# Optimization experiments

Hardware: AMD Instinct MI355X
Metric: run time of the kernel (lower is better)

## Reference

```python
import jax, jax.numpy as jnp
import numpy as np

V, H, L, BW = 32000, 512, 2, 5   # vocab, hidden(=embed), gru layers, beam width
NEG = -1e9                        # -inf surrogate for duplicate initial beams


def gru_cell(x, h, Wi, Wh, bi, bh):
    # PyTorch GRU gate order: r, z, n.  x:[B,H] h:[B,H] Wi,Wh:[3H,H]
    gi = x @ Wi.T + bi
    gh = h @ Wh.T + bh
    ir, iz, inn = jnp.split(gi, 3, axis=-1)
    hr, hz, hn = jnp.split(gh, 3, axis=-1)
    r = jax.nn.sigmoid(ir + hr)
    z = jax.nn.sigmoid(iz + hz)
    n = jnp.tanh(inn + r * hn)
    return (1.0 - z) * n + z * h


def setup_inputs() -> dict:
    key = jax.random.key(0)
    ks = jax.random.split(key, 14)
    s = 0.05
    p = lambda k, shape: jax.random.normal(k, shape, jnp.float32) * s
    return {
        "input_seq": jax.random.randint(ks[0], (128, 1), 0, V),
        "input_length": 128,
        "max_length": 64,
        "SOS_token": 1,
        "emb": p(ks[1], (V, H)),
        "enc_Wi": p(ks[2], (L, 3 * H, H)),
        "enc_Wh": p(ks[3], (L, 3 * H, H)),
        "enc_bi": p(ks[4], (L, 3 * H)),
        "enc_bh": p(ks[5], (L, 3 * H)),
        "dec_Wi": p(ks[6], (L, 3 * H, H)),
        "dec_Wh": p(ks[7], (L, 3 * H, H)),
        "dec_bi": p(ks[8], (L, 3 * H)),
        "dec_bh": p(ks[9], (L, 3 * H)),
        "Wc": p(ks[10], (H, 2 * H)),
        "bc": p(ks[11], (H,)),
        "Wout": p(ks[12], (V, H)),
        "bout": p(ks[13], (V,)),
    }


def reference(input_seq, input_length, max_length, SOS_token,
              emb, enc_Wi, enc_Wh, enc_bi, enc_bh,
              dec_Wi, dec_Wh, dec_bi, dec_bh, Wc, bc, Wout, bout):
    # ---- encoder: L-layer GRU over [T,1] token ids ----
    x = emb[input_seq[:, 0]]                    # [T,H]

    def enc_step(h, xt):                        # h:[L,1,H]
        inp = xt[None]                          # [1,H]
        hs = []
        for l in range(L):
            hl = gru_cell(inp, h[l], enc_Wi[l], enc_Wh[l], enc_bi[l], enc_bh[l])
            hs.append(hl)
            inp = hl
        return jnp.stack(hs), inp[0]

    h0 = jnp.zeros((L, 1, H), x.dtype)
    enc_hidden, enc_out = jax.lax.scan(enc_step, h0, x)   # enc_out:[T,H]

    # ---- one decoder step, batched over all BW beams ----
    def dec_step(tokens, hidden):               # tokens:[BW] hidden:[L,BW,H]
        inp = emb[tokens]                       # [BW,H]
        hs = []
        for l in range(L):
            hl = gru_cell(inp, hidden[l], dec_Wi[l], dec_Wh[l], dec_bi[l], dec_bh[l])
            hs.append(hl)
            inp = hl
        rnn = inp                               # [BW,H] top-layer output
        e = jnp.einsum('bh,th->bt', rnn, enc_out)          # Luong dot scores
        a = jax.nn.softmax(e, axis=-1)
        ctx = a @ enc_out                       # [BW,H]
        cc = jnp.tanh(jnp.concatenate([rnn, ctx], axis=-1) @ Wc.T + bc)
        logits = cc @ Wout.T + bout             # [BW,V]
        return logits, jnp.stack(hs)

    # ---- beam search: all beams in one batched decoder call per step ----
    tokens0 = jnp.full((BW,), SOS_token, jnp.int32)
    hid0 = jnp.broadcast_to(enc_hidden, (L, BW, H))
    scores0 = jnp.full((BW,), NEG, jnp.float32).at[0].set(0.0)  # one live beam

    def step(carry, _):
        tokens, hidden, scores = carry
        logits, hidden = dec_step(tokens, hidden)
        logp = jax.nn.log_softmax(logits, axis=-1)
        top_lp, top_idx = jax.lax.top_k(logp, BW)            # [BW,BW]
        cand = (scores[:, None] + top_lp).reshape(-1)        # [BW*BW]
        sc, flat = jax.lax.top_k(cand, BW)
        parent = flat // BW
        new_tok = top_idx.reshape(-1)[flat]
        hidden = hidden[:, parent, :]
        return (new_tok, hidden, sc), (new_tok, parent)

    (_, _, final_scores), (toks, pars) = jax.lax.scan(
        step, (tokens0, hid0, scores0), None, length=max_length)

    # ---- backtrack best hypothesis through parent pointers ----
    best = jnp.argmax(final_scores)

    def back(beam, tp):
        t, p = tp
        return p[beam], t[beam]

    _, seq = jax.lax.scan(back, best, (toks, pars), reverse=True)
    return seq, final_scores[best]
```

## Files before the change

kernel.cpp:

```cpp
#include <hip/hip_runtime.h>
#include <math.h>

#define VV 32000
#define HH 512
#define G3 1536
#define TI 128
#define TO 64
#define NB 5
#define NEGF (-1000000000.0f)
#define NTHR 256
#define NT5 512
#define NCH 500
#define LSTR 32

struct Params {
  const int* seq;
  const int* sosp;
  const float *emb, *eWi, *eWh, *ebi, *ebh;
  const float *dWi, *dWh, *dbi, *dbh;
  const float *Wc, *bc, *Wout, *bout;
  unsigned* bar;
  int *cur_tok, *toks, *pars, *ptop_i;
  float *gi0, *eout, *h0b, *h1b, *dch, *cc, *ptop_v, *psum, *scores;
  float* out;
};

__device__ __forceinline__ float cldf(const float* p) {
  return __hip_atomic_load(p, __ATOMIC_RELAXED, __HIP_MEMORY_SCOPE_AGENT);
}
__device__ __forceinline__ void cstf(float* p, float v) {
  __hip_atomic_store(p, v, __ATOMIC_RELAXED, __HIP_MEMORY_SCOPE_AGENT);
}
__device__ __forceinline__ int cldi(const int* p) {
  return __hip_atomic_load(p, __ATOMIC_RELAXED, __HIP_MEMORY_SCOPE_AGENT);
}
__device__ __forceinline__ void csti(int* p, int v) {
  __hip_atomic_store(p, v, __ATOMIC_RELAXED, __HIP_MEMORY_SCOPE_AGENT);
}
__device__ __forceinline__ unsigned rldu(const unsigned* p) {
  return __hip_atomic_load(p, __ATOMIC_RELAXED, __HIP_MEMORY_SCOPE_AGENT);
}
typedef unsigned long long u64t;
union F2U { u64t u; float f[2]; };
__device__ __forceinline__ void cld2(float* d, const float* p) {
  F2U x; x.u = __hip_atomic_load((const u64t*)p, __ATOMIC_RELAXED, __HIP_MEMORY_SCOPE_AGENT);
  d[0] = x.f[0]; d[1] = x.f[1];
}

__device__ __forceinline__ void bar_arrive(unsigned* lines, int myline) {
  __syncthreads();
  if (threadIdx.x == 0)
    __hip_atomic_fetch_add(lines + myline * LSTR, 1u,
                           __ATOMIC_RELAXED, __HIP_MEMORY_SCOPE_AGENT);
}
template <int SLP>
__device__ __forceinline__ void bar_wait8(const unsigned* lines, unsigned tgt) {
  if (threadIdx.x < 64) {
    for (;;) {
      unsigned v = tgt;
      if (threadIdx.x < 8) v = rldu(lines + threadIdx.x * LSTR);
      if (__all(v >= tgt)) break;
      __builtin_amdgcn_s_sleep(SLP);
    }
  }
  __syncthreads();
}
__device__ __forceinline__ void bcast_store(unsigned* L, int NL, unsigned tok) {
  asm volatile("s_waitcnt vmcnt(0)" ::: "memory");
  for (int i = 0; i < NL; i++)
    __hip_atomic_store(L + i * LSTR, tok, __ATOMIC_RELAXED, __HIP_MEMORY_SCOPE_AGENT);
}
template <int SLP>
__device__ __forceinline__ void leaf_wait(const unsigned* L, int grp, unsigned tok) {
  if (threadIdx.x == 0) {
    while (rldu(L + grp * LSTR) < tok) __builtin_amdgcn_s_sleep(SLP);
  }
  __syncthreads();
}

__device__ __forceinline__ float wredf(float v) {
#pragma unroll
  for (int o = 32; o; o >>= 1) v += __shfl_xor(v, o, 64);
  return v;
}

__global__ void __launch_bounds__(NTHR) k_e0(Params p) {
  const int wg = blockIdx.x, tid = threadIdx.x;
  const int lane = tid & 63, wv = tid >> 6;
  if (wg == 0) {
    for (int i = tid; i < 2 * HH; i += NTHR) { cstf(&p.h0b[i], 0.f); cstf(&p.h1b[i], 0.f); }
  }
  for (int lr = 0; lr < 6; lr++) {
    int row = wg * 6 + lr;
    const float* W = p.eWi + (size_t)row * HH;
    float w0[8];
#pragma unroll
    for (int j = 0; j < 8; j++) w0[j] = W[j * 64 + lane];
    float bi = p.ebi[row];
    for (int t = wv; t < TI; t += 4) {
      const float* x = p.emb + (size_t)p.seq[t] * HH;
      float s = 0.f;
#pragma unroll
      for (int j = 0; j < 8; j++) s += w0[j] * x[j * 64 + lane];
      s = wredf(s);
      if (lane == 0) p.gi0[(size_t)t * G3 + row] = s + bi;
    }
  }
}

__device__ void enc_step(const Params& p, int T, int wg, int lane, int wv) {
  const int sIn = T & 1, sOut = sIn ^ 1;
  if (wv < 2) {
    if (T < TI) {
      float hv[8];
#pragma unroll
      for (int j = 0; j < 8; j++) hv[j] = cldf(&p.h0b[sIn * HH + j * 64 + lane]);
#pragma unroll
      for (int uu = 0; uu < 4; uu++) {
        int u = wg * 8 + wv * 4 + uu;
        float g[3];
#pragma unroll
        for (int gg = 0; gg < 3; gg++) {
          const float* W = p.eWh + (size_t)(gg * HH + u) * HH;
          float s = 0.f;
#pragma unroll
          for (int j = 0; j < 8; j++) s += W[j * 64 + lane] * hv[j];
          g[gg] = wredf(s);
        }
        if (lane == 0) {
          const float* gr = p.gi0 + (size_t)T * G3;
          float ir = gr[u], iz = gr[HH + u], inn = gr[2 * HH + u];
          float hr = g[0] + p.ebh[u], hz = g[1] + p.ebh[HH + u], hn = g[2] + p.ebh[2 * HH + u];
          float r = 1.f / (1.f + expf(-(ir + hr)));
          float z = 1.f / (1.f + expf(-(iz + hz)));
          float n = tanhf(inn + r * hn);
          float hp = cldf(&p.h0b[sIn * HH + u]);
          cstf(&p.h0b[sOut * HH + u], (1.f - z) * n + z * hp);
        }
      }
    }
  } else {
    if (T >= 1) {
      float xv[8], hv[8];
#pragma unroll
      for (int j = 0; j < 8; j++) {
        xv[j] = cldf(&p.h0b[sIn * HH + j * 64 + lane]);
        hv[j] = cldf(&p.h1b[sOut * HH + j * 64 + lane]);
      }
#pragma unroll
      for (int uu = 0; uu < 4; uu++) {
        int u = wg * 8 + (wv - 2) * 4 + uu;
        float gi[3], gh[3];
#pragma unroll
        for (int gg = 0; gg < 3; gg++) {
          const float* Wi1 = p.eWi + (size_t)G3 * HH + (size_t)(gg * HH + u) * HH;
          const float* Wh1 = p.eWh + (size_t)G3 * HH + (size_t)(gg * HH + u) * HH;
          float si = 0.f, s2 = 0.f;
#pragma unroll
          for (int j = 0; j < 8; j++) { si += Wi1[j * 64 + lane] * xv[j]; s2 += Wh1[j * 64 + lane] * hv[j]; }
          gi[gg] = wredf(si);
          gh[gg] = wredf(s2);
        }
        if (lane == 0) {
          const float* bi = p.ebi + G3;
          const float* bh = p.ebh + G3;
          float ir = gi[0] + bi[u], iz = gi[1] + bi[HH + u], inn = gi[2] + bi[2 * HH + u];
          float hr = gh[0] + bh[u], hz = gh[1] + bh[HH + u], hn = gh[2] + bh[2 * HH + u];
          float r = 1.f / (1.f + expf(-(ir + hr)));
          float z = 1.f / (1.f + expf(-(iz + hz)));
          float n = tanhf(inn + r * hn);
          float hp = cldf(&p.h1b[sOut * HH + u]);
          float hnew = (1.f - z) * n + z * hp;
          cstf(&p.h1b[sIn * HH + u], hnew);
          p.eout[(size_t)(T - 1) * HH + u] = hnew;
        }
      }
    }
  }
}

__global__ void __launch_bounds__(NTHR) k_e1x2(Params p, int k) {
  const int wg = blockIdx.x, tid = threadIdx.x;
  const int lane = tid & 63, wv = tid >> 6;
  unsigned* ceA = p.bar + 0 * LSTR;
  enc_step(p, 2 * k, wg, lane, wv);
  if (2 * k + 1 <= TI) {
    bar_arrive(ceA, wg & 7);
    bar_wait8<2>(ceA, (unsigned)(8 * (k + 1)));
    enc_step(p, 2 * k + 1, wg, lane, wv);
  }
}

__global__ void __launch_bounds__(NTHR) k_d0(Params p) {
  const int wg = blockIdx.x, tid = threadIdx.x;
  for (int i = tid + wg * NTHR; i < 2 * NB * HH; i += 64 * NTHR) {
    int l = i / (NB * HH);
    int rem = i - l * (NB * HH);
    int u = rem % HH;
    p.dch[(size_t)l * NB * HH + rem] = (l == 0) ? cldf(&p.h0b[u]) : cldf(&p.h1b[u]);
  }
  if (wg == 0 && tid < NB) {
    p.cur_tok[tid] = p.sosp[0];
    p.scores[tid] = (tid == 0) ? 0.f : NEGF;
  }
}

template <int LAYER>
__device__ void gru_body(const Params& p, float* sm, int t, int ib, int ob,
                         int wg, int tid, int lane, int wv) {
  float* sx = sm;
  float* sh = sm + NB * HH;
  float* fres = sm + 2 * NB * HH;
  int ct[NB], pr[NB];
#pragma unroll
  for (int b = 0; b < NB; b++) {
    ct[b] = (LAYER == 0) ? cldi(&p.cur_tok[b]) : 0;
    pr[b] = (t == 0) ? b : cldi(&p.pars[(t - 1) * NB + b]);
  }
  for (int i = tid; i < NB * (HH / 2); i += NTHR) {
    int b = i >> 8, c = (i & 255) << 1;
    float x2[2], h2[2];
    if (LAYER == 0) {
      const float* e = p.emb + (size_t)ct[b] * HH + c;
      x2[0] = e[0]; x2[1] = e[1];
    } else {
      cld2(x2, &p.dch[((size_t)(ob * 2 + 0) * NB + b) * HH + c]);
    }
    cld2(h2, &p.dch[((size_t)(ib * 2 + LAYER) * NB + pr[b]) * HH + c]);
    sx[b * HH + c] = x2[0]; sx[b * HH + c + 1] = x2[1];
    sh[b * HH + c] = h2[0]; sh[b * HH + c + 1] = h2[1];
  }
  __syncthreads();
  const float* Wi = p.dWi + (size_t)LAYER * G3 * HH;
  const float* Wh = p.dWh + (size_t)LAYER * G3 * HH;
#pragma unroll
  for (int k = 0; k < 12; k++) {
    const int m_ = k % 6;
    const int f = wv * 12 + k;
    const int ul = f / 6;
    const int u = wg * 8 + ul;
    const float* W = (m_ >= 3 ? Wh : Wi) + (size_t)((m_ % 3) * HH + u) * HH;
    const float* vecb = (m_ >= 3) ? sh : sx;
    float wd[8];
#pragma unroll
    for (int j = 0; j < 8; j++) wd[j] = W[j * 64 + lane];
    float a0 = 0.f, a1 = 0.f, a2 = 0.f, a3 = 0.f, a4 = 0.f;
#pragma unroll
    for (int j = 0; j < 8; j++) {
      float wj = wd[j];
      int o = j * 64 + lane;
      a0 += wj * vecb[0 * HH + o];
      a1 += wj * vecb[1 * HH + o];
      a2 += wj * vecb[2 * HH + o];
      a3 += wj * vecb[3 * HH + o];
      a4 += wj * vecb[4 * HH + o];
    }
    float r0 = wredf(a0), r1 = wredf(a1), r2 = wredf(a2), r3 = wredf(a3), r4 = wredf(a4);
    if (lane == 0) {
      fres[f * NB + 0] = r0; fres[f * NB + 1] = r1; fres[f * NB + 2] = r2;
      fres[f * NB + 3] = r3; fres[f * NB + 4] = r4;
    }
  }
  __syncthreads();
  if (tid < 8 * NB) {
    int ul = tid / NB, b = tid - ul * NB;
    int u = wg * 8 + ul;
    const float* bi = p.dbi + LAYER * G3;
    const float* bh = p.dbh + LAYER * G3;
    float ir = fres[(ul * 6 + 0) * NB + b] + bi[u];
    float iz = fres[(ul * 6 + 1) * NB + b] + bi[HH + u];
    float inn = fres[(ul * 6 + 2) * NB + b] + bi[2 * HH + u];
    float hr = fres[(ul * 6 + 3) * NB + b] + bh[u];
    float hz = fres[(ul * 6 + 4) * NB + b] + bh[HH + u];
    float hn = fres[(ul * 6 + 5) * NB + b] + bh[2 * HH + u];
    float hp = sh[b * HH + u];
    float r = 1.f / (1.f + expf(-(ir + hr)));
    float z = 1.f / (1.f + expf(-(iz + hz)));
    float n = tanhf(inn + r * hn);
    cstf(&p.dch[((size_t)(ob * 2 + LAYER) * NB + b) * HH + u], (1.f - z) * n + z * hp);
  }
  __syncthreads();
}

__global__ void __launch_bounds__(NTHR) k_gru2(Params p, int t) {
  const int wg = blockIdx.x, tid = threadIdx.x;
  const int lane = tid & 63, wv = tid >> 6;
  const int ib = t & 1, ob = ib ^ 1;
  __shared__ float sm[2 * NB * HH + 48 * NB];
  unsigned* gruA = p.bar + 8 * LSTR;
  gru_body<0>(p, sm, t, ib, ob, wg, tid, lane, wv);
  bar_arrive(gruA, wg & 7);
  bar_wait8<2>(gruA, (unsigned)(8 * (t + 1)));
  gru_body<1>(p, sm, t, ib, ob, wg, tid, lane, wv);
}

__global__ void __launch_bounds__(NT5) k_pa56(Params p, int t) {
  const int wg = blockIdx.x, tid = threadIdx.x;
  const int lane = tid & 63, wv = tid >> 6;
  const int ob = (t & 1) ^ 1;
  __shared__ float sm[5760];
  __shared__ unsigned s_mrg;
  unsigned* paA = p.bar + 16 * LSTR;
  unsigned* paF = p.bar + 24 * LSTR;
  unsigned* c5A = p.bar + 48 * LSTR;
  unsigned* c5F = p.bar + 56 * LSTR;
  unsigned* paL = p.bar + 64 * LSTR;

  if (wg < 40) {
    const int b = wg / 8, q = wg % 8;
    float* srnn = sm;
    float* sp = sm + 512;
    float* cpart = sm + 640;
    float* sctx = sm + 4736;
    for (int i = tid; i < HH; i += NT5)
      srnn[i] = cldf(&p.dch[((size_t)(ob * 2 + 1) * NB + b) * HH + i]);
    __syncthreads();
    for (int j = wv; j < TI; j += 8) {
      const float* E = p.eout + (size_t)j * HH;
      float s = 0.f;
#pragma unroll
      for (int k2 = 0; k2 < 8; k2++) s += srnn[k2 * 64 + lane] * E[k2 * 64 + lane];
      s = wredf(s);
      if (lane == 0) sp[j] = s;
    }
    __syncthreads();
    if (wv == 0) {
      float v0 = sp[lane], v1 = sp[64 + lane];
      float mx = fmaxf(v0, v1);
#pragma unroll
      for (int o = 32; o; o >>= 1) mx = fmaxf(mx, __shfl_xor(mx, o, 64));
      float e0 = expf(v0 - mx), e1 = expf(v1 - mx);
      float ss = wredf(e0 + e1);
      sp[lane] = e0 / ss;
      sp[64 + lane] = e1 / ss;
    }
    __syncthreads();
    {
      float cp[8];
#pragma unroll
      for (int k2 = 0; k2 < 8; k2++) cp[k2] = 0.f;
      for (int j = wv; j < TI; j += 8) {
        float spj = sp[j];
        const float* E = p.eout + (size_t)j * HH;
#pragma unroll
        for (int k2 = 0; k2 < 8; k2++) cp[k2] += spj * E[k2 * 64 + lane];
      }
#pragma unroll
      for (int k2 = 0; k2 < 8; k2++) cpart[wv * HH + k2 * 64 + lane] = cp[k2];
    }
    __syncthreads();
    for (int i = tid; i < HH; i += NT5)
      sctx[i] = ((cpart[0 * HH + i] + cpart[1 * HH + i]) + (cpart[2 * HH + i] + cpart[3 * HH + i]))
              + ((cpart[4 * HH + i] + cpart[5 * HH + i]) + (cpart[6 * HH + i] + cpart[7 * HH + i]));
    __syncthreads();
    for (int k = wv; k < 64; k += 8) {
      int u = q * 64 + k;
      const float* W = p.Wc + (size_t)u * (2 * HH);
      float s0 = 0.f, s1 = 0.f;
#pragma unroll
      for (int j = 0; j < 8; j++) {
        int o = j * 64 + lane;
        s0 += W[o] * srnn[o];
        s1 += W[HH + o] * sctx[o];
      }
      float r0 = wredf(s0), r1 = wredf(s1);
      if (lane == 0) cstf(&p.cc[b * HH + u], tanhf(r0 + r1 + p.bc[u]));
    }
    __syncthreads();
    if (tid == 0) {
      unsigned o1 = __hip_atomic_fetch_add(paA + (wg & 7) * LSTR, 1u,
                                           __ATOMIC_RELAXED, __HIP_MEMORY_SCOPE_AGENT);
      if (o1 == (unsigned)(5 * (t + 1) - 1)) {
        unsigned o2 = __hip_atomic_fetch_add(paF, 1u,
                                             __ATOMIC_RELAXED, __HIP_MEMORY_SCOPE_AGENT);
        if (o2 == (unsigned)(8 * (t + 1) - 1))
          bcast_store(paL, 32, (unsigned)(t + 1));
      }
    }
  }
  leaf_wait<4>(paL, wg >> 4, (unsigned)(t + 1));

  {
    float* scc = sm;
    float* slg = sm + 2560;
    float* part = sm + 2944;
    for (int i = tid; i < NB * (HH / 2); i += NT5) {
      int b = i >> 8, c = (i & 255) << 1;
      float c2v[2];
      cld2(c2v, &p.cc[b * HH + c]);
      scc[b * HH + c] = c2v[0]; scc[b * HH + c + 1] = c2v[1];
    }
    __syncthreads();
    const int vbase = wg * 64;
    {
      const int e = tid >> 6, r = tid & 63;
      const float4* Wr = (const float4*)(p.Wout + (size_t)(vbase + r) * HH + e * 64);
      const float* sc0 = scc + e * 64;
      float a0 = 0.f, a1 = 0.f, a2 = 0.f, a3 = 0.f, a4 = 0.f;
#pragma unroll
      for (int c = 0; c < 16; c++) {
        float4 w = Wr[c];
        const float4 s0 = *(const float4*)(sc0 + 0 * HH + 4 * c);
        const float4 s1 = *(const float4*)(sc0 + 1 * HH + 4 * c);
        const float4 s2 = *(const float4*)(sc0 + 2 * HH + 4 * c);
        const float4 s3 = *(const float4*)(sc0 + 3 * HH + 4 * c);
        const float4 s4 = *(const float4*)(sc0 + 4 * HH + 4 * c);
        a0 += ((w.x * s0.x + w.y * s0.y) + (w.z * s0.z + w.w * s0.w));
        a1 += ((w.x * s1.x + w.y * s1.y) + (w.z * s1.z + w.w * s1.w));
        a2 += ((w.x * s2.x + w.y * s2.y) + (w.z * s2.z + w.w * s2.w));
        a3 += ((w.x * s3.x + w.y * s3.y) + (w.z * s3.z + w.w * s3.w));
        a4 += ((w.x * s4.x + w.y * s4.y) + (w.z * s4.z + w.w * s4.w));
      }
      float* pt = part + (size_t)tid * NB;
      pt[0] = a0; pt[1] = a1; pt[2] = a2; pt[3] = a3; pt[4] = a4;
    }
    __syncthreads();
    if (tid < 64) {
      float bo = p.bout[vbase + tid];
#pragma unroll
      for (int b = 0; b < NB; b++) {
        float s01 = part[(size_t)(0 * 64 + tid) * NB + b] + part[(size_t)(1 * 64 + tid) * NB + b];
        float s23 = part[(size_t)(2 * 64 + tid) * NB + b] + part[(size_t)(3 * 64 + tid) * NB + b];
        float s45 = part[(size_t)(4 * 64 + tid) * NB + b] + part[(size_t)(5 * 64 + tid) * NB + b];
        float s67 = part[(size_t)(6 * 64 + tid) * NB + b] + part[(size_t)(7 * 64 + tid) * NB + b];
        slg[b * 64 + tid] = ((s01 + s23) + (s45 + s67)) + bo;
      }
    }
    __syncthreads();
    if (wv == 0) {
      for (int b = 0; b < NB; b++) {
        float s0 = expf(slg[b * 64 + lane]);
        float ss = wredf(s0);
        if (lane == 0) cstf(&p.psum[wg * NB + b], ss);
      }
    } else if (wv == 1 && lane < NB) {
      int b = lane;
      float bv[5]; int bidx[5];
#pragma unroll
      for (int k = 0; k < 5; k++) { bv[k] = -INFINITY; bidx[k] = 0x7fffffff; }
      for (int r = 0; r < 64; r++) {
        float v = slg[b * 64 + r];
        if (v > bv[4]) {
          int k = 4;
          while (k > 0 && v > bv[k - 1]) { bv[k] = bv[k - 1]; bidx[k] = bidx[k - 1]; k--; }
          bv[k] = v; bidx[k] = vbase + r;
        }
      }
#pragma unroll
      for (int k = 0; k < 5; k++) {
        cstf(&p.ptop_v[(wg * NB + b) * 5 + k], bv[k]);
        csti(&p.ptop_i[(wg * NB + b) * 5 + k], bidx[k]);
      }
    }
  }

  __syncthreads();
  if (tid == 0) {
    unsigned m = 0;
    const unsigned cnt = ((wg & 7) < 4) ? 63u : 62u;
    unsigned o1 = __hip_atomic_fetch_add(c5A + (wg & 7) * LSTR, 1u,
                                         __ATOMIC_RELAXED, __HIP_MEMORY_SCOPE_AGENT);
    if (o1 == cnt * (unsigned)(t + 1) - 1u) {
      unsigned o2 = __hip_atomic_fetch_add(c5F, 1u,
                                           __ATOMIC_RELAXED, __HIP_MEMORY_SCOPE_AGENT);
      if (o2 == (unsigned)(8 * (t + 1) - 1)) m = 1;
    }
    s_mrg = m;
  }
  __syncthreads();

  if (s_mrg) {
    float* sls = sm;
    float* smv = sm + 8;
    int* smi = (int*)(sm + 40);
    for (int b = wv; b < NB; b += 8) {
      float qsum = 0.f;
#pragma unroll
      for (int g = 0; g < 8; g++) {
        int w = lane + g * 64;
        qsum += (w < NCH) ? cldf(&p.psum[(size_t)w * NB + b]) : 0.f;
      }
      float ssum = wredf(qsum);
      float bv[5]; int bix[5];
#pragma unroll
      for (int k = 0; k < 5; k++) { bv[k] = -INFINITY; bix[k] = 0x7fffffff; }
      for (int g = 0; g < 8; g++) {
        int w = lane + g * 64;
        if (w < NCH) {
#pragma unroll
          for (int k = 0; k < 5; k++) {
            float v = cldf(&p.ptop_v[((size_t)w * NB + b) * 5 + k]);
            int id = cldi(&p.ptop_i[((size_t)w * NB + b) * 5 + k]);
            if (v > bv[4] || (v == bv[4] && id < bix[4])) {
              int kk = 4;
              while (kk > 0 && (v > bv[kk - 1] || (v == bv[kk - 1] && id < bix[kk - 1]))) {
                bv[kk] = bv[kk - 1]; bix[kk] = bix[kk - 1]; kk--;
              }
              bv[kk] = v; bix[kk] = id;
            }
          }
        }
      }
#pragma unroll
      for (int off = 1; off < 64; off <<= 1) {
        float ov[5]; int oi[5];
#pragma unroll
        for (int k = 0; k < 5; k++) { ov[k] = __shfl_xor(bv[k], off, 64); oi[k] = __shfl_xor(bix[k], off, 64); }
        float nv[5]; int ni[5];
        int i2 = 0, j2 = 0;
#pragma unroll
        for (int k = 0; k < 5; k++) {
          bool ta = (bv[i2] > ov[j2]) || (bv[i2] == ov[j2] && bix[i2] < oi[j2]);
          if (ta) { nv[k] = bv[i2]; ni[k] = bix[i2]; i2++; }
          else { nv[k] = ov[j2]; ni[k] = oi[j2]; j2++; }
        }
#pragma unroll
        for (int k = 0; k < 5; k++) { bv[k] = nv[k]; bix[k] = ni[k]; }
      }
      if (lane == 0) {
        sls[b] = logf(ssum);
#pragma unroll
        for (int k = 0; k < 5; k++) { smv[b * 5 + k] = bv[k]; smi[b * 5 + k] = bix[k]; }
      }
    }
    __syncthreads();
    if (tid == 0) {
      float cand[25]; int ctok[25];
      for (int b = 0; b < NB; b++) {
        float sb = cldf(&p.scores[b]), lb = sls[b];
#pragma unroll
        for (int k = 0; k < 5; k++) {
          cand[b * 5 + k] = sb + (smv[b * 5 + k] - lb);
          ctok[b * 5 + k] = smi[b * 5 + k];
        }
      }
      float s5[5]; int f5[5];
#pragma unroll
      for (int k = 0; k < 5; k++) { s5[k] = -INFINITY; f5[k] = 0x7fffffff; }
      for (int f = 0; f < 25; f++) {
        float v = cand[f];
        if (v > s5[4]) {
          int k = 4;
          while (k > 0 && v > s5[k - 1]) { s5[k] = s5[k - 1]; f5[k] = f5[k - 1]; k--; }
          s5[k] = v; f5[k] = f;
        }
      }
      for (int j2 = 0; j2 < 5; j2++) {
        int fl = f5[j2];
        csti(&p.pars[t * NB + j2], fl / 5);
        csti(&p.toks[t * NB + j2], ctok[fl]);
        csti(&p.cur_tok[j2], ctok[fl]);
      }
      for (int j2 = 0; j2 < 5; j2++) cstf(&p.scores[j2], s5[j2]);
      if (t == TO - 1) {
        int best = 0;
        float bvv = s5[0];
        for (int j = 1; j < NB; j++)
          if (s5[j] > bvv) { bvv = s5[j]; best = j; }
        int beam = best;
        for (int tt = TO - 1; tt >= 0; tt--) {
          p.out[tt] = (float)cldi(&p.toks[tt * NB + beam]);
          beam = cldi(&p.pars[tt * NB + beam]);
        }
        p.out[TO] = bvv;
      }
    }
  }
}

extern "C" void kernel_launch(void* const* d_in, const int* in_sizes, int n_in,
                              void* d_out, int out_size, void* d_ws, size_t ws_size,
                              hipStream_t stream) {
  (void)in_sizes; (void)n_in; (void)out_size; (void)ws_size;
  Params p;
  p.seq  = (const int*)d_in[0];
  p.sosp = (const int*)d_in[3];
  p.emb  = (const float*)d_in[4];
  p.eWi  = (const float*)d_in[5];
  p.eWh  = (const float*)d_in[6];
  p.ebi  = (const float*)d_in[7];
  p.ebh  = (const float*)d_in[8];
  p.dWi  = (const float*)d_in[9];
  p.dWh  = (const float*)d_in[10];
  p.dbi  = (const float*)d_in[11];
  p.dbh  = (const float*)d_in[12];
  p.Wc   = (const float*)d_in[13];
  p.bc   = (const float*)d_in[14];
  p.Wout = (const float*)d_in[15];
  p.bout = (const float*)d_in[16];

  char* w = (char*)d_ws;
  size_t off = 0;
  auto alloc = [&](size_t words) -> char* {
    char* r = w + off;
    off += words * 4;
    off = (off + 255) & ~(size_t)255;
    return r;
  };
  p.bar     = (unsigned*)alloc(96 * LSTR);
  p.cur_tok = (int*)alloc(8);
  p.toks    = (int*)alloc(TO * NB);
  p.pars    = (int*)alloc(TO * NB);
  p.ptop_i  = (int*)alloc(NCH * NB * 5);
  p.gi0     = (float*)alloc((size_t)TI * G3);
  p.eout    = (float*)alloc((size_t)TI * HH);
  p.h0b     = (float*)alloc(2 * HH);
  p.h1b     = (float*)alloc(2 * HH);
  p.dch     = (float*)alloc(2 * 2 * NB * HH);
  p.cc      = (float*)alloc(NB * HH);
  p.ptop_v  = (float*)alloc(NCH * NB * 5);
  p.psum    = (float*)alloc(NCH * NB);
  p.scores  = (float*)alloc(8);
  p.out     = (float*)d_out;

  (void)hipMemsetAsync(d_ws, 0, 96 * LSTR * 4, stream);

  k_e0<<<dim3(256), dim3(NTHR), 0, stream>>>(p);
  for (int k = 0; k <= TI / 2; k++)
    k_e1x2<<<dim3(64), dim3(NTHR), 0, stream>>>(p, k);
  k_d0<<<dim3(64), dim3(NTHR), 0, stream>>>(p);
  for (int t = 0; t < TO; t++) {
    k_gru2<<<dim3(64), dim3(NTHR), 0, stream>>>(p, t);
    k_pa56<<<dim3(NCH), dim3(NT5), 0, stream>>>(p, t);
  }
}
```

Baseline: 7.197 ms.

## Compute output logits per-wave with coalesced row reads and wave reductions

Reorganizes the vocab-projection dot products so each wave handles 8 full rows of Wout, with lanes reading contiguous float4 chunks (coalesced) and reducing across the wave. The beam context vectors are held in registers instead of re-read from LDS per row. This removes the LDS partial-sum buffer and one barrier, and the original pattern, where each thread read a 256-byte slice of one row, was poorly coalesced. In exchange it needs more cross-lane shuffle reductions (5 per row) and more registers.

Result: no change. 7.182 ms (-0.2%).

```diff
diff --git a/kernel.cpp b/kernel.cpp
--- a/kernel.cpp
+++ b/kernel.cpp
@@ -383,7 +383,6 @@
   {
     float* scc = sm;
     float* slg = sm + 2560;
-    float* part = sm + 2944;
     for (int i = tid; i < NB * (HH / 2); i += NT5) {
       int b = i >> 8, c = (i & 255) << 1;
       float c2v[2];
@@ -392,38 +391,30 @@
     }
     __syncthreads();
     const int vbase = wg * 64;
-    {
-      const int e = tid >> 6, r = tid & 63;
-      const float4* Wr = (const float4*)(p.Wout + (size_t)(vbase + r) * HH + e * 64);
-      const float* sc0 = scc + e * 64;
-      float a0 = 0.f, a1 = 0.f, a2 = 0.f, a3 = 0.f, a4 = 0.f;
-#pragma unroll
-      for (int c = 0; c < 16; c++) {
-        float4 w = Wr[c];
-        const float4 s0 = *(const float4*)(sc0 + 0 * HH + 4 * c);
-        const float4 s1 = *(const float4*)(sc0 + 1 * HH + 4 * c);
-        const float4 s2 = *(const float4*)(sc0 + 2 * HH + 4 * c);
-        const float4 s3 = *(const float4*)(sc0 + 3 * HH + 4 * c);
-        const float4 s4 = *(const float4*)(sc0 + 4 * HH + 4 * c);
-        a0 += ((w.x * s0.x + w.y * s0.y) + (w.z * s0.z + w.w * s0.w));
-        a1 += ((w.x * s1.x + w.y * s1.y) + (w.z * s1.z + w.w * s1.w));
-        a2 += ((w.x * s2.x + w.y * s2.y) + (w.z * s2.z + w.w * s2.w));
-        a3 += ((w.x * s3.x + w.y * s3.y) + (w.z * s3.z + w.w * s3.w));
-        a4 += ((w.x * s4.x + w.y * s4.y) + (w.z * s4.z + w.w * s4.w));
-      }
-      float* pt = part + (size_t)tid * NB;
-      pt[0] = a0; pt[1] = a1; pt[2] = a2; pt[3] = a3; pt[4] = a4;
-    }
-    __syncthreads();
-    if (tid < 64) {
-      float bo = p.bout[vbase + tid];
+    float4 sb0[NB], sb1[NB];
+#pragma unroll
+    for (int b = 0; b < NB; b++) {
+      sb0[b] = *(const float4*)(scc + b * HH + 4 * lane);
+      sb1[b] = *(const float4*)(scc + b * HH + 256 + 4 * lane);
+    }
+#pragma unroll
+    for (int rr = 0; rr < 8; rr++) {
+      const int rl = wv * 8 + rr;
+      const float4* W4 = (const float4*)(p.Wout + (size_t)(vbase + rl) * HH);
+      float4 w0 = W4[lane];
+      float4 w1 = W4[64 + lane];
+      float d[NB];
 #pragma unroll
       for (int b = 0; b < NB; b++) {
-        float s01 = part[(size_t)(0 * 64 + tid) * NB + b] + part[(size_t)(1 * 64 + tid) * NB + b];
-        float s23 = part[(size_t)(2 * 64 + tid) * NB + b] + part[(size_t)(3 * 64 + tid) * NB + b];
-        float s45 = part[(size_t)(4 * 64 + tid) * NB + b] + part[(size_t)(5 * 64 + tid) * NB + b];
-        float s67 = part[(size_t)(6 * 64 + tid) * NB + b] + part[(size_t)(7 * 64 + tid) * NB + b];
-        slg[b * 64 + tid] = ((s01 + s23) + (s45 + s67)) + bo;
+        d[b] = ((w0.x * sb0[b].x + w0.y * sb0[b].y) + (w0.z * sb0[b].z + w0.w * sb0[b].w))
+             + ((w1.x * sb1[b].x + w1.y * sb1[b].y) + (w1.z * sb1[b].z + w1.w * sb1[b].w));
+      }
+#pragma unroll
+      for (int b = 0; b < NB; b++) d[b] = wredf(d[b]);
+      if (lane == 0) {
+        float bo = p.bout[vbase + rl];
+#pragma unroll
+        for (int b = 0; b < NB; b++) slg[b * 64 + rl] = d[b] + bo;
       }
     }
     __syncthreads();
```
